# Performance work log

Measured on AMD Instinct MI355X. Metric: run time of the kernel, lower is better.

## Reference

```python
import jax, jax.numpy as jnp
import numpy as np

B, N, F, U, K = 8, 2048, 128, 128, 3
NEG = -1.0e9


def setup_inputs() -> dict:
    key = jax.random.key(0)
    k1, k2, k3, k4, k5 = jax.random.split(key, 5)
    x = jax.random.normal(k1, (B, N, F), dtype=jnp.float32)
    # symmetric binary adjacency, density ~0.005 (avg degree ~20)
    m = (jax.random.uniform(k2, (N, N)) < 0.005).astype(jnp.float32)
    adj = jnp.maximum(m, m.T)
    s_w = np.sqrt(2.0 / (F + U)).astype(np.float32)   # glorot normal
    s_a = np.sqrt(2.0 / (U + N)).astype(np.float32)
    w = jax.random.normal(k3, (K, F, U), dtype=jnp.float32) * s_w
    ai = jax.random.normal(k4, (U, N), dtype=jnp.float32) * s_a
    aj = jax.random.normal(k5, (U, N), dtype=jnp.float32) * s_a
    return {"x": x, "adj": adj, "w": w, "ai": ai, "aj": aj}


def reference(x, adj, w, ai, aj):
    n = adj.shape[0]
    A = adj + jnp.eye(n, dtype=adj.dtype)          # adj + I (self loops)
    A_abs = jnp.abs(A)
    # hop 0
    f = jnp.einsum('bnf,fu->bnu', x, w[0])          # [B,N,U]
    attn = jnp.einsum('bnu,um->bnm', f, ai) \
         + jnp.swapaxes(jnp.einsum('bnu,um->bnm', f, aj), 1, 2)  # [B,N,N]
    attn = attn + NEG * (1.0 - A_abs)
    attn = jax.nn.softmax(attn, axis=1) * A
    a = attn
    # hops 1..k-1
    for i in range(1, w.shape[0]):
        h = jnp.einsum('bnf,bnm->bmf', x, a)        # (x^T @ a)^T, [B,N,F]
        f = jnp.einsum('bmf,fu->bmu', h, w[i]) + f
        a = jnp.matmul(a, attn)
    return jax.nn.relu(f), attn
```

## Files before the change

kernel.cpp:

```cpp
#include <hip/hip_runtime.h>
#include <math.h>

#define B 8
#define N 2048
#define F 128
#define U 128
#define CAP 64


typedef unsigned int uint;
typedef unsigned short ushort;

using short8 = __attribute__((ext_vector_type(8))) short;
using f32x4v = __attribute__((ext_vector_type(4))) float;

__device__ inline ushort f2bf(float v) {
  uint u = __float_as_uint(v);
  u += 0x7fffu + ((u >> 16) & 1u);
  return (ushort)(u >> 16);
}
__device__ inline float bflo(uint p) { return __uint_as_float(p << 16); }
__device__ inline float bfhi(uint p) { return __uint_as_float(p & 0xffff0000u); }

__global__ __launch_bounds__(256) void prep_kernel(
    const float* __restrict__ x, const float* __restrict__ w0,
    const float* __restrict__ ai, const float* __restrict__ aj,
    const float* __restrict__ adj, ushort* __restrict__ f0h,
    ushort* __restrict__ g1h, ushort* __restrict__ g2h,
    float* __restrict__ aiT, ushort* __restrict__ ajTh,
    int* __restrict__ col_idx, int* __restrict__ col_cnt,
    int* __restrict__ col_diag) {
  __shared__ ushort wT[128 * 136];
  const int blk = blockIdx.x;
  const int tid = threadIdx.x;
  if (blk < 512) {
    const int block_row = blk * 32;
    const int wv = tid >> 6, lane = tid & 63;
    const int rt = wv & 1, cg = wv >> 1;
    const int rowbase = block_row + rt * 16;
    const int arow = rowbase + (lane & 15);
    const int asl = (lane >> 4) * 8;
    short8 afr[4];
#pragma unroll
    for (int kk = 0; kk < 4; kk++) {
      const int k0 = kk * 32 + asl;
      float4 xa = *(const float4*)(x + (size_t)arow * F + k0);
      float4 xb = *(const float4*)(x + (size_t)arow * F + k0 + 4);
      afr[kk][0] = (short)f2bf(xa.x); afr[kk][1] = (short)f2bf(xa.y);
      afr[kk][2] = (short)f2bf(xa.z); afr[kk][3] = (short)f2bf(xa.w);
      afr[kk][4] = (short)f2bf(xb.x); afr[kk][5] = (short)f2bf(xb.y);
      afr[kk][6] = (short)f2bf(xb.z); afr[kk][7] = (short)f2bf(xb.w);
    }
    const int crow = rowbase + ((lane >> 4) << 2);
    for (int h = 0; h < 3; h++) {
      __syncthreads();
      for (int idx = tid; idx < 128 * 128; idx += 256) {
        int k = idx >> 7, n = idx & 127;
        wT[n * 136 + k] = f2bf(w0[h * 16384 + idx]);
      }
      __syncthreads();
      f32x4v acc[4];
#pragma unroll
      for (int ct = 0; ct < 4; ct++) acc[ct] = (f32x4v){0.f, 0.f, 0.f, 0.f};
#pragma unroll
      for (int kk = 0; kk < 4; kk++) {
        const int k0 = kk * 32 + asl;
#pragma unroll
        for (int ct = 0; ct < 4; ct++) {
          const int col = cg * 64 + ct * 16 + (lane & 15);
          short8 b = *(const short8*)&wT[col * 136 + k0];
          acc[ct] =
              __builtin_amdgcn_mfma_f32_16x16x32_bf16(afr[kk], b, acc[ct], 0, 0, 0);
        }
      }
      ushort* dst = (h == 0) ? f0h : (h == 1) ? g1h : g2h;
#pragma unroll
      for (int ct = 0; ct < 4; ct++) {
        const int ccol = cg * 64 + ct * 16 + (lane & 15);
#pragma unroll
        for (int r = 0; r < 4; r++)
          dst[(size_t)(crow + r) * U + ccol] = f2bf(acc[ct][r]);
      }
    }
  } else if (blk < 1024) {
    const int m = (blk - 512) * 4 + (tid >> 6);
    const int lane = tid & 63;
    const float* row = adj + (size_t)m * N;
    int cnt = 0;
    int dflag = 0;
    for (int base = 0; base < N; base += 64) {
      int n = base + lane;
      float v = row[n];
      if ((n == m) && (v != 0.f)) dflag = 1;
      bool pred = (v != 0.f) && (n != m);
      unsigned long long mask = __ballot(pred);
      if (pred) {
        int off = cnt + (int)__popcll(mask & ((1ull << lane) - 1ull));
        if (off < CAP - 1) col_idx[m * CAP + off] = n;
      }
      cnt += (int)__popcll(mask);
    }
    unsigned long long dm = __ballot(dflag != 0);
    if (lane == 0) {
      col_cnt[m] = cnt > CAP - 1 ? CAP - 1 : cnt;
      col_diag[m] = dm ? 1 : 0;
    }
  } else {
    int idx = (blk - 1024) * 256 + tid;
    int n = idx >> 7;
    int u = idx & 127;
    aiT[idx] = ai[u * N + n];
    ajTh[idx] = f2bf(aj[u * N + n]);
  }
}

__global__ __launch_bounds__(256) void attn_u_kernel(
    const ushort* __restrict__ f0h, const float* __restrict__ aiT,
    const ushort* __restrict__ ajTh, const ushort* __restrict__ g1h,
    const ushort* __restrict__ g2h, const int* __restrict__ col_idx,
    const int* __restrict__ col_cnt, const int* __restrict__ col_diag,
    float* __restrict__ attn, float* __restrict__ col_val,
    float* __restrict__ dval, ushort* __restrict__ uh) {
  const int wid = (blockIdx.x << 2) + (threadIdx.x >> 6);
  const int lane = threadIdx.x & 63;
  const int b = wid >> 11;
  const int m = wid & 2047;
  const int cnt = col_cnt[m];
  float* attnb = attn + (size_t)b * N * N;
  float* cv = col_val + ((size_t)b * N + m) * CAP;
  const ushort* g2b = g2h + (size_t)b * N * F;
  const size_t oh = ((size_t)b * N + m) * F + 2 * lane;
  const uint g1r = *(const uint*)(g1h + oh);

  if (col_diag[m]) {
    if (lane < cnt) cv[lane] = 0.f;
    if (lane == 0) {
      dval[b * N + m] = 2.f;
      attnb[(size_t)m * N + m] = 2.f;
    }
    uint g2r = *(const uint*)(g2b + m * F + 2 * lane);
    float a0 = bflo(g1r) + 2.f * bflo(g2r);
    float a1 = bfhi(g1r) + 2.f * bfhi(g2r);
    *(uint*)(uh + oh) = (uint)f2bf(a0) | ((uint)f2bf(a1) << 16);
    return;
  }

  const int g = lane >> 4;
  const int s = lane & 15;
  const int nent = cnt + 1;
  const float4 aim0 = *(const float4*)(aiT + m * U + s * 8);
  const float4 aim1 = *(const float4*)(aiT + m * U + s * 8 + 4);
  const uint4 fmv = *(const uint4*)(f0h + ((size_t)b * N + m) * U + s * 8);
  const float fm0 = bflo(fmv.x), fm1 = bfhi(fmv.x);
  const float fm2 = bflo(fmv.y), fm3 = bfhi(fmv.y);
  const float fm4 = bflo(fmv.z), fm5 = bfhi(fmv.z);
  const float fm6 = bflo(fmv.w), fm7 = bfhi(fmv.w);

  float q_own = -INFINITY;
  int n_own = m;
  float mx = -INFINITY;
  for (int jj = 0; jj * 4 < nent; jj++) {
    const int e = jj * 4 + g;
    float q = -INFINITY;
    int n = m;
    if (e < nent) {
      n = (e == 0) ? m : col_idx[m * CAP + e - 1];
      uint4 fn = *(const uint4*)(f0h + ((size_t)b * N + n) * U + s * 8);
      uint4 an = *(const uint4*)(ajTh + n * U + s * 8);
      q = bflo(fn.x) * aim0.x + bfhi(fn.x) * aim0.y + bflo(fn.y) * aim0.z +
          bfhi(fn.y) * aim0.w + bflo(fn.z) * aim1.x + bfhi(fn.z) * aim1.y +
          bflo(fn.w) * aim1.z + bfhi(fn.w) * aim1.w + fm0 * bflo(an.x) +
          fm1 * bfhi(an.x) + fm2 * bflo(an.y) + fm3 * bfhi(an.y) +
          fm4 * bflo(an.z) + fm5 * bfhi(an.z) + fm6 * bflo(an.w) +
          fm7 * bfhi(an.w);
    }
    q += __shfl_xor(q, 1, 64);
    q += __shfl_xor(q, 2, 64);
    q += __shfl_xor(q, 4, 64);
    q += __shfl_xor(q, 8, 64);
    mx = fmaxf(mx, q);
    if (s == jj) { q_own = q; n_own = n; }
  }
  mx = fmaxf(mx, __shfl_xor(mx, 16, 64));
  mx = fmaxf(mx, __shfl_xor(mx, 32, 64));
  float e_own = expf(q_own - mx);
  float ssum = e_own;
  ssum += __shfl_xor(ssum, 1, 64);
  ssum += __shfl_xor(ssum, 2, 64);
  ssum += __shfl_xor(ssum, 4, 64);
  ssum += __shfl_xor(ssum, 8, 64);
  ssum += __shfl_xor(ssum, 16, 64);
  ssum += __shfl_xor(ssum, 32, 64);
  const float v_own = e_own / ssum;
  const int eo = s * 4 + g;
  if (eo < nent) {
    if (eo == 0) {
      dval[b * N + m] = v_own;
      attnb[(size_t)m * N + m] = v_own;
    } else {
      cv[eo - 1] = v_own;
      attnb[(size_t)n_own * N + m] = v_own;
    }
  }
  float a0 = bflo(g1r), a1 = bfhi(g1r);
  float b0 = 0.f, b1 = 0.f;
  int e = 0;
  for (; e + 1 < nent; e += 2) {
    int src0 = ((e & 3) << 4) + (e >> 2);
    int src1 = (((e + 1) & 3) << 4) + ((e + 1) >> 2);
    float v0 = __shfl(v_own, src0, 64);
    int n0 = __shfl(n_own, src0, 64);
    float v1 = __shfl(v_own, src1, 64);
    int n1 = __shfl(n_own, src1, 64);
    uint gx0 = *(const uint*)(g2b + n0 * F + 2 * lane);
    uint gx1 = *(const uint*)(g2b + n1 * F + 2 * lane);
    a0 += v0 * bflo(gx0);
    a1 += v0 * bfhi(gx0);
    b0 += v1 * bflo(gx1);
    b1 += v1 * bfhi(gx1);
  }
  if (e < nent) {
    int src = ((e & 3) << 4) + (e >> 2);
    float v = __shfl(v_own, src, 64);
    int n = __shfl(n_own, src, 64);
    uint gx = *(const uint*)(g2b + n * F + 2 * lane);
    a0 += v * bflo(gx);
    a1 += v * bfhi(gx);
  }
  a0 += b0;
  a1 += b1;
  *(uint*)(uh + oh) = (uint)f2bf(a0) | ((uint)f2bf(a1) << 16);
}

__global__ __launch_bounds__(256) void spmm_out_kernel(
    const ushort* __restrict__ uh, const ushort* __restrict__ f0h,
    const int* __restrict__ col_idx, const int* __restrict__ col_cnt,
    const float* __restrict__ col_val, const float* __restrict__ dval,
    float* __restrict__ out) {
  const int wid = (blockIdx.x << 2) + (threadIdx.x >> 6);
  const int lane = threadIdx.x & 63;
  const int b = wid >> 11;
  const int m = wid & 2047;
  const ushort* inb = uh + (size_t)b * N * F;
  const int cnt = col_cnt[m];
  const float* cv = col_val + ((size_t)b * N + m) * CAP;
  const float dv = dval[b * N + m];
  uint vm = *(const uint*)(inb + m * F + 2 * lane);
  float a0 = dv * bflo(vm);
  float a1 = dv * bfhi(vm);
  float c0 = 0.f, c1 = 0.f;
  int j = 0;
  for (; j + 1 < cnt; j += 2) {
    int n0 = col_idx[m * CAP + j];
    int n1 = col_idx[m * CAP + j + 1];
    float v0 = cv[j];
    float v1 = cv[j + 1];
    uint g0 = *(const uint*)(inb + n0 * F + 2 * lane);
    uint g1 = *(const uint*)(inb + n1 * F + 2 * lane);
    a0 += v0 * bflo(g0);
    a1 += v0 * bfhi(g0);
    c0 += v1 * bflo(g1);
    c1 += v1 * bfhi(g1);
  }
  if (j < cnt) {
    int n = col_idx[m * CAP + j];
    float v = cv[j];
    uint g = *(const uint*)(inb + n * F + 2 * lane);
    a0 += v * bflo(g);
    a1 += v * bfhi(g);
  }
  a0 += c0;
  a1 += c1;
  const size_t o = ((size_t)b * N + m) * F + 2 * lane;
  const uint f0r = *(const uint*)(f0h + o);
  float2 ov;
  ov.x = fmaxf(bflo(f0r) + a0, 0.f);
  ov.y = fmaxf(bfhi(f0r) + a1, 0.f);
  *(float2*)(out + o) = ov;
}

extern "C" void kernel_launch(void* const* d_in, const int* in_sizes, int n_in,
                              void* d_out, int out_size, void* d_ws,
                              size_t ws_size, hipStream_t stream) {
  const float* x = (const float*)d_in[0];
  const float* adj = (const float*)d_in[1];
  const float* w = (const float*)d_in[2];
  const float* ai = (const float*)d_in[3];
  const float* aj = (const float*)d_in[4];

  float* out_f = (float*)d_out;
  float* out_attn = out_f + (size_t)B * N * U;

  char* p = (char*)d_ws;
  float* aiT = (float*)p;     p += (size_t)N * U * 4;
  float* col_val = (float*)p; p += (size_t)B * N * CAP * 4;
  float* dval = (float*)p;    p += (size_t)B * N * 4;
  int* col_idx = (int*)p;     p += (size_t)N * CAP * 4;
  int* col_cnt = (int*)p;     p += (size_t)N * 4;
  int* col_diag = (int*)p;    p += (size_t)N * 4;
  ushort* f0h = (ushort*)p;   p += (size_t)B * N * U * 2;
  ushort* ajTh = (ushort*)p;  p += (size_t)N * U * 2;
  ushort* g1h = (ushort*)p;   p += (size_t)B * N * U * 2;
  ushort* g2h = (ushort*)p;   p += (size_t)B * N * U * 2;
  ushort* uh = (ushort*)p;    p += (size_t)B * N * U * 2;

  prep_kernel<<<2048, 256, 0, stream>>>(x, w, ai, aj, adj, f0h, g1h, g2h, aiT,
                                        ajTh, col_idx, col_cnt, col_diag);
  attn_u_kernel<<<B * N / 4, 256, 0, stream>>>(
      f0h, aiT, ajTh, g1h, g2h, col_idx, col_cnt, col_diag, out_attn, col_val,
      dval, uh);
  spmm_out_kernel<<<B * N / 4, 256, 0, stream>>>(uh, f0h, col_idx, col_cnt,
                                                 col_val, dval, out_f);
}
```

Before: 79.87 us.

## Fuse softmax and neighbor gather into one pass; unroll SpMM by four

The attention kernel now does the softmax and the weighted gather of g2 rows in a single loop over neighbor chunks. It accumulates unnormalized exp-weighted sums and divides by the total once at the end. This drops the max-subtraction pass and the separate serialized gather loop that needed per-entry shuffles. It risks exp overflow if logits grow large, since there is no max stabilization, and it adds extra loads for padded entries. The output SpMM kernel is also unrolled to four independent accumulators to expose more memory-level parallelism.

```diff
diff --git a/kernel.cpp b/kernel.cpp
--- a/kernel.cpp
+++ b/kernel.cpp
@@ -156,79 +156,68 @@
   const float fm4 = bflo(fmv.z), fm5 = bfhi(fmv.z);
   const float fm6 = bflo(fmv.w), fm7 = bfhi(fmv.w);
 
+  float ssum = 0.f;
+  float ua0 = 0.f, ua1 = 0.f, ub0 = 0.f, ub1 = 0.f;
+  float uc0 = 0.f, uc1 = 0.f, ud0 = 0.f, ud1 = 0.f;
   float q_own = -INFINITY;
   int n_own = m;
-  float mx = -INFINITY;
-  for (int jj = 0; jj * 4 < nent; jj++) {
+  const int niter = (nent + 3) >> 2;
+#pragma unroll 2
+  for (int jj = 0; jj < niter; jj++) {
     const int e = jj * 4 + g;
-    float q = -INFINITY;
+    const bool valid = e < nent;
     int n = m;
-    if (e < nent) {
-      n = (e == 0) ? m : col_idx[m * CAP + e - 1];
-      uint4 fn = *(const uint4*)(f0h + ((size_t)b * N + n) * U + s * 8);
-      uint4 an = *(const uint4*)(ajTh + n * U + s * 8);
-      q = bflo(fn.x) * aim0.x + bfhi(fn.x) * aim0.y + bflo(fn.y) * aim0.z +
-          bfhi(fn.y) * aim0.w + bflo(fn.z) * aim1.x + bfhi(fn.z) * aim1.y +
-          bflo(fn.w) * aim1.z + bfhi(fn.w) * aim1.w + fm0 * bflo(an.x) +
-          fm1 * bfhi(an.x) + fm2 * bflo(an.y) + fm3 * bfhi(an.y) +
-          fm4 * bflo(an.z) + fm5 * bfhi(an.z) + fm6 * bflo(an.w) +
-          fm7 * bfhi(an.w);
-    }
+    if (valid && e > 0) n = col_idx[m * CAP + e - 1];
+    const int n0 = __shfl(n, 0, 64);
+    const int n1 = __shfl(n, 16, 64);
+    const int n2 = __shfl(n, 32, 64);
+    const int n3 = __shfl(n, 48, 64);
+    const uint gx0 = *(const uint*)(g2b + n0 * F + 2 * lane);
+    const uint gx1 = *(const uint*)(g2b + n1 * F + 2 * lane);
+    const uint gx2 = *(const uint*)(g2b + n2 * F + 2 * lane);
+    const uint gx3 = *(const uint*)(g2b + n3 * F + 2 * lane);
+    const uint4 fn = *(const uint4*)(f0h + ((size_t)b * N + n) * U + s * 8);
+    const uint4 an = *(const uint4*)(ajTh + n * U + s * 8);
+    float q = bflo(fn.x) * aim0.x + bfhi(fn.x) * aim0.y + bflo(fn.y) * aim0.z +
+              bfhi(fn.y) * aim0.w + bflo(fn.z) * aim1.x + bfhi(fn.z) * aim1.y +
+              bflo(fn.w) * aim1.z + bfhi(fn.w) * aim1.w + fm0 * bflo(an.x) +
+              fm1 * bfhi(an.x) + fm2 * bflo(an.y) + fm3 * bfhi(an.y) +
+              fm4 * bflo(an.z) + fm5 * bfhi(an.z) + fm6 * bflo(an.w) +
+              fm7 * bfhi(an.w);
     q += __shfl_xor(q, 1, 64);
     q += __shfl_xor(q, 2, 64);
     q += __shfl_xor(q, 4, 64);
     q += __shfl_xor(q, 8, 64);
-    mx = fmaxf(mx, q);
+    if (!valid) q = -INFINITY;
     if (s == jj) { q_own = q; n_own = n; }
-  }
-  mx = fmaxf(mx, __shfl_xor(mx, 16, 64));
-  mx = fmaxf(mx, __shfl_xor(mx, 32, 64));
-  float e_own = expf(q_own - mx);
-  float ssum = e_own;
-  ssum += __shfl_xor(ssum, 1, 64);
-  ssum += __shfl_xor(ssum, 2, 64);
-  ssum += __shfl_xor(ssum, 4, 64);
-  ssum += __shfl_xor(ssum, 8, 64);
-  ssum += __shfl_xor(ssum, 16, 64);
-  ssum += __shfl_xor(ssum, 32, 64);
-  const float v_own = e_own / ssum;
+    const float q0 = __shfl(q, 0, 64);
+    const float q1 = __shfl(q, 16, 64);
+    const float q2 = __shfl(q, 32, 64);
+    const float q3 = __shfl(q, 48, 64);
+    const float e0 = expf(q0);
+    const float e1 = expf(q1);
+    const float e2 = expf(q2);
+    const float e3 = expf(q3);
+    ssum += (e0 + e1) + (e2 + e3);
+    ua0 += e0 * bflo(gx0); ua1 += e0 * bfhi(gx0);
+    ub0 += e1 * bflo(gx1); ub1 += e1 * bfhi(gx1);
+    uc0 += e2 * bflo(gx2); uc1 += e2 * bfhi(gx2);
+    ud0 += e3 * bflo(gx3); ud1 += e3 * bfhi(gx3);
+  }
+  const float inv = 1.f / ssum;
   const int eo = s * 4 + g;
   if (eo < nent) {
+    const float v = expf(q_own) * inv;
     if (eo == 0) {
-      dval[b * N + m] = v_own;
-      attnb[(size_t)m * N + m] = v_own;
+      dval[b * N + m] = v;
+      attnb[(size_t)m * N + m] = v;
     } else {
-      cv[eo - 1] = v_own;
-      attnb[(size_t)n_own * N + m] = v_own;
-    }
-  }
-  float a0 = bflo(g1r), a1 = bfhi(g1r);
-  float b0 = 0.f, b1 = 0.f;
-  int e = 0;
-  for (; e + 1 < nent; e += 2) {
-    int src0 = ((e & 3) << 4) + (e >> 2);
-    int src1 = (((e + 1) & 3) << 4) + ((e + 1) >> 2);
-    float v0 = __shfl(v_own, src0, 64);
-    int n0 = __shfl(n_own, src0, 64);
-    float v1 = __shfl(v_own, src1, 64);
-    int n1 = __shfl(n_own, src1, 64);
-    uint gx0 = *(const uint*)(g2b + n0 * F + 2 * lane);
-    uint gx1 = *(const uint*)(g2b + n1 * F + 2 * lane);
-    a0 += v0 * bflo(gx0);
-    a1 += v0 * bfhi(gx0);
-    b0 += v1 * bflo(gx1);
-    b1 += v1 * bfhi(gx1);
-  }
-  if (e < nent) {
-    int src = ((e & 3) << 4) + (e >> 2);
-    float v = __shfl(v_own, src, 64);
-    int n = __shfl(n_own, src, 64);
-    uint gx = *(const uint*)(g2b + n * F + 2 * lane);
-    a0 += v * bflo(gx);
-    a1 += v * bfhi(gx);
-  }
-  a0 += b0;
-  a1 += b1;
+      cv[eo - 1] = v;
+      attnb[(size_t)n_own * N + m] = v;
+    }
+  }
+  const float a0 = bflo(g1r) + inv * ((ua0 + ub0) + (uc0 + ud0));
+  const float a1 = bfhi(g1r) + inv * ((ua1 + ub1) + (uc1 + ud1));
   *(uint*)(uh + oh) = (uint)f2bf(a0) | ((uint)f2bf(a1) << 16);
 }
 
@@ -248,29 +237,32 @@
   uint vm = *(const uint*)(inb + m * F + 2 * lane);
   float a0 = dv * bflo(vm);
   float a1 = dv * bfhi(vm);
-  float c0 = 0.f, c1 = 0.f;
+  float b0 = 0.f, b1 = 0.f, c0 = 0.f, c1 = 0.f, d0 = 0.f, d1 = 0.f;
   int j = 0;
-  for (; j + 1 < cnt; j += 2) {
+  for (; j + 3 < cnt; j += 4) {
     int n0 = col_idx[m * CAP + j];
     int n1 = col_idx[m * CAP + j + 1];
-    float v0 = cv[j];
-    float v1 = cv[j + 1];
+    int n2 = col_idx[m * CAP + j + 2];
+    int n3 = col_idx[m * CAP + j + 3];
+    float v0 = cv[j], v1 = cv[j + 1], v2 = cv[j + 2], v3 = cv[j + 3];
     uint g0 = *(const uint*)(inb + n0 * F + 2 * lane);
     uint g1 = *(const uint*)(inb + n1 * F + 2 * lane);
-    a0 += v0 * bflo(g0);
-    a1 += v0 * bfhi(g0);
-    c0 += v1 * bflo(g1);
-    c1 += v1 * bfhi(g1);
-  }
-  if (j < cnt) {
+    uint g2 = *(const uint*)(inb + n2 * F + 2 * lane);
+    uint g3 = *(const uint*)(inb + n3 * F + 2 * lane);
+    a0 += v0 * bflo(g0); a1 += v0 * bfhi(g0);
+    b0 += v1 * bflo(g1); b1 += v1 * bfhi(g1);
+    c0 += v2 * bflo(g2); c1 += v2 * bfhi(g2);
+    d0 += v3 * bflo(g3); d1 += v3 * bfhi(g3);
+  }
+  for (; j < cnt; j++) {
     int n = col_idx[m * CAP + j];
     float v = cv[j];
     uint g = *(const uint*)(inb + n * F + 2 * lane);
     a0 += v * bflo(g);
     a1 += v * bfhi(g);
   }
-  a0 += c0;
-  a1 += c1;
+  a0 += b0 + c0 + d0;
+  a1 += b1 + c1 + d1;
   const size_t o = ((size_t)b * N + m) * F + 2 * lane;
   const uint f0r = *(const uint*)(f0h + o);
   float2 ov;
```

New measurement: 81.60 us. 2.2% more time.
